# Kernel optimization log

Measured on AMD Instinct MI355X. Metric: run time of the kernel, lower is better.

The kernel has to match this reference:

```python
import jax, jax.numpy as jnp
import numpy as np
import math

CHANNELS, BINS, HEADS, KSIZE = 4, 1024, 8, 3
ROT_DIM = BINS // HEADS // 2  # 64: rotate first half of each 128-dim head


def _rope(t):
    # t: [b, c, heads, w, d]; rotate first ROT_DIM dims, interleaved-pair style
    w = t.shape[-2]
    inv_freq = 1.0 / (10000.0 ** (jnp.arange(0, ROT_DIM, 2, dtype=jnp.float32) / ROT_DIM))
    freqs = jnp.arange(w, dtype=jnp.float32)[:, None] * inv_freq[None, :]   # [w, ROT_DIM//2]
    freqs = jnp.repeat(freqs, 2, axis=-1)                                    # [w, ROT_DIM]
    cos, sin = jnp.cos(freqs), jnp.sin(freqs)
    t_rot, t_pass = t[..., :ROT_DIM], t[..., ROT_DIM:]
    pair = t_rot.reshape(t_rot.shape[:-1] + (ROT_DIM // 2, 2))
    rotated = jnp.stack((-pair[..., 1], pair[..., 0]), axis=-1).reshape(t_rot.shape)
    return jnp.concatenate([t_rot * cos + rotated * sin, t_pass], axis=-1)


def _proj(x, w_lin, w_conv, b_conv):
    # MultichannelLinear: contract last dim with per-channel [out, in] weight
    y = jnp.einsum('bchi,coi->bcho', x, w_lin)
    # depthwise Conv2d, kernel (1, 3), padding (0, 1), groups = channels
    y = jax.lax.conv_general_dilated(
        y, w_conv, window_strides=(1, 1), padding=((0, 0), (1, 1)),
        dimension_numbers=('NCHW', 'OIHW', 'NCHW'), feature_group_count=CHANNELS)
    return y + b_conv[None, :, None, None]


def _split_heads(y):
    b, c, h, w = y.shape
    # transpose(2,3) -> [b,c,w,h]; reshape -> [b,c,w,heads,d]; permute -> [b,c,heads,w,d]
    return y.transpose(0, 1, 3, 2).reshape(b, c, w, HEADS, h // HEADS).transpose(0, 1, 3, 2, 4)


def setup_inputs() -> dict:
    key = jax.random.key(0)
    k1, k2, k3, k4, k5 = jax.random.split(key, 5)
    s_lin = 1.0 / math.sqrt(BINS)
    x = jax.random.normal(k1, (2, CHANNELS, BINS, BINS), dtype=jnp.float32)
    w_q_lin = jax.random.uniform(k2, (CHANNELS, BINS, BINS), jnp.float32, -s_lin, s_lin)
    w_q_conv = jax.random.uniform(k3, (CHANNELS, 1, 1, KSIZE), jnp.float32, -0.5, 0.5)
    b_q_conv = jax.random.uniform(k4, (CHANNELS,), jnp.float32, -0.5, 0.5)
    w_out = jax.random.uniform(k5, (CHANNELS, BINS, BINS), jnp.float32, -s_lin, s_lin)
    return {"x": x, "w_q_lin": w_q_lin, "w_q_conv": w_q_conv, "b_q_conv": b_q_conv, "w_out": w_out}


def reference(x, w_q_lin, w_q_conv, b_q_conv, w_out):
    b, c, h, w = x.shape
    # NOTE: original forward uses self.q_proj for q, k AND v (k_proj/v_proj unused)
    p = _proj(x, w_q_lin, w_q_conv, b_q_conv)          # [b,c,h,w]
    ph = _split_heads(p)                                # [b,c,heads,w,d]
    q = _rope(ph)
    k = _rope(ph)
    v = ph
    qk = jnp.einsum('bcnqd,bcnkd->bcnqk', q, k) / math.sqrt(h)
    a = jnp.einsum('bcnqk,bcnkd->bcnqd', jax.nn.softmax(qk, axis=-1), v)
    # merge heads back: [b,c,heads,w,d] -> [b,c,w,h] -> [b,c,h,w]
    a = a.transpose(0, 1, 3, 2, 4).reshape(b, c, w, h).transpose(0, 1, 3, 2)
    return jnp.einsum('bchi,coi->bcho', a, w_out)
```

## Files before the change

### kernel.cpp

```cpp
#include <hip/hip_runtime.h>
#include <cstdint>
#include <cstddef>

typedef __bf16 bf16;
typedef bf16 bf16x4 __attribute__((ext_vector_type(4)));
typedef bf16 bf16x8 __attribute__((ext_vector_type(8)));
typedef float f32x4 __attribute__((ext_vector_type(4)));

__device__ __forceinline__ void gload_lds16(const bf16* g, bf16* l) {
    __builtin_amdgcn_global_load_lds(
        (__attribute__((address_space(1))) void*)(uintptr_t)(g),
        (__attribute__((address_space(3))) void*)(l),
        16, 0, 0);
}

__global__ __launch_bounds__(256) void cvt_kernel(const float* __restrict__ in,
                                                  bf16* __restrict__ out, int n4) {
    int i = blockIdx.x * 256 + threadIdx.x;
    if (i >= n4) return;
    float4 v = ((const float4*)in)[i];
    bf16x4 o;
    o[0] = (bf16)v.x; o[1] = (bf16)v.y; o[2] = (bf16)v.z; o[3] = (bf16)v.w;
    *(bf16x4*)(out + (size_t)i * 4) = o;
}

__global__ __launch_bounds__(256) void rope_tab_kernel(float2* __restrict__ t) {
    int i = blockIdx.x * 256 + threadIdx.x;
    int w = i >> 5, j = i & 31;
    float inv = exp2f(-(float)j * (13.287712379549449f / 32.0f));
    float a = (float)w * inv;
    t[i] = make_float2(cosf(a), sinf(a));
}

template <bool F32OUT>
__global__ void __launch_bounds__(256) gemm_bt(const bf16* __restrict__ A,
                                               const bf16* __restrict__ B,
                                               void* __restrict__ Cout) {
    __shared__ alignas(16) bf16 As[128 * 64];
    __shared__ alignas(16) bf16 Bs[128 * 64];
    const int tid = threadIdx.x, lane = tid & 63, wave = tid >> 6;
    const int l15 = lane & 15, quad = lane >> 4;
    const int s = blockIdx.z;
    const bf16* Ab = A + ((size_t)s << 20) + (size_t)blockIdx.y * 128 * 1024;
    const bf16* Bb = B + ((size_t)(s & 3) << 20) + (size_t)blockIdx.x * 128 * 1024;
    const int wm = (wave >> 1) * 64, wn = (wave & 1) * 64;

    const f32x4 fzero = {0.f, 0.f, 0.f, 0.f};
    f32x4 acc[4][4];
    for (int i = 0; i < 4; ++i)
        for (int j = 0; j < 4; ++j) acc[i][j] = fzero;

    const int sr = wave * 8 + (lane >> 3);
    const int sc = (lane & 7) * 8;

    for (int kt = 0; kt < 16; ++kt) {
        __syncthreads();
        for (int it = 0; it < 4; ++it) {
            int r = it * 32 + sr;
            gload_lds16(Ab + (size_t)r * 1024 + kt * 64 + sc, As + r * 64 + sc);
            gload_lds16(Bb + (size_t)r * 1024 + kt * 64 + sc, Bs + r * 64 + sc);
        }
        __syncthreads();
        for (int kk = 0; kk < 2; ++kk) {
            bf16x8 af[4], bfr[4];
            for (int i = 0; i < 4; ++i)
                af[i] = *(const bf16x8*)(As + (wm + i * 16 + l15) * 64 + kk * 32 + quad * 8);
            for (int j = 0; j < 4; ++j)
                bfr[j] = *(const bf16x8*)(Bs + (wn + j * 16 + l15) * 64 + kk * 32 + quad * 8);
            for (int i = 0; i < 4; ++i)
                for (int j = 0; j < 4; ++j)
                    acc[i][j] = __builtin_amdgcn_mfma_f32_16x16x32_bf16(af[i], bfr[j],
                                                                        acc[i][j], 0, 0, 0);
        }
    }
    size_t cbase = ((size_t)s << 20) + (size_t)blockIdx.y * 128 * 1024 + blockIdx.x * 128;
    for (int i = 0; i < 4; ++i)
        for (int j = 0; j < 4; ++j) {
            int m = wm + i * 16 + quad * 4;
            int n = wn + j * 16 + l15;
            for (int r = 0; r < 4; ++r) {
                float v = acc[i][j][r];
                if (F32OUT)
                    ((float*)Cout)[cbase + (size_t)(m + r) * 1024 + n] = v;
                else
                    ((bf16*)Cout)[cbase + (size_t)(m + r) * 1024 + n] = (bf16)v;
            }
        }
}

__global__ void __launch_bounds__(256) conv_rope_kernel(
    const bf16* __restrict__ Yb, const float* __restrict__ wconv,
    const float* __restrict__ bconv, bf16* __restrict__ Qhat,
    bf16* __restrict__ Vhat, const float2* __restrict__ rtab) {
    __shared__ float Pt[32][260];
    const int s = blockIdx.z, cch = s & 3;
    const int h0 = blockIdx.y * 32, w0 = blockIdx.x * 256;
    const bf16* Y = Yb + ((size_t)s << 20);
    const float k0 = wconv[cch * 3], k1 = wconv[cch * 3 + 1], k2 = wconv[cch * 3 + 2];
    const float bias = bconv[cch];

    for (int it = 0; it < 4; ++it) {
        const int hh = threadIdx.x >> 3;
        const int wseg = (threadIdx.x & 7) + it * 8;
        const int h = h0 + hh, w = w0 + wseg * 8;
        const bf16* yrow = Y + ((size_t)h << 10);
        bf16x8 yv = *(const bf16x8*)(yrow + w);
        float yc[10];
        yc[0] = (w > 0) ? (float)yrow[w - 1] : 0.f;
        for (int i = 0; i < 8; ++i) yc[i + 1] = (float)yv[i];
        yc[9] = (w + 8 < 1024) ? (float)yrow[w + 8] : 0.f;
        bf16x8 pb;
        for (int i = 0; i < 8; ++i) {
            float p = fmaf(k0, yc[i], fmaf(k1, yc[i + 1], fmaf(k2, yc[i + 2], bias)));
            Pt[hh][wseg * 8 + i] = p;
            pb[i] = (bf16)p;
        }
        const int head = h >> 7, d = h & 127;
        *(bf16x8*)(Vhat + ((((size_t)s * 8 + head) * 128 + (w >> 3)) << 10) + d * 8) = pb;
    }
    __syncthreads();
    {
        const int dcb = threadIdx.x >> 6;
        const int head = h0 >> 7;
        const int d0 = (h0 & 127) + dcb * 8;
        const int hb0 = dcb * 8;
        for (int it = 0; it < 4; ++it) {
            const int wl = (threadIdx.x & 63) + it * 64;
            const int w = w0 + wl;
            float q[8];
            if (d0 < 64) {
                for (int j = 0; j < 8; j += 2) {
                    float2 cs = rtab[(w << 5) + ((d0 + j) >> 1)];
                    float a = Pt[hb0 + j][wl], b = Pt[hb0 + j + 1][wl];
                    q[j]     = fmaf(a, cs.x, -b * cs.y);
                    q[j + 1] = fmaf(b, cs.x,  a * cs.y);
                }
            } else {
                for (int j = 0; j < 8; ++j) q[j] = Pt[hb0 + j][wl];
            }
            bf16x8 qb;
            for (int j = 0; j < 8; ++j) qb[j] = (bf16)q[j];
            *(bf16x8*)(Qhat + ((((size_t)s * 8 + head) * 16 + (d0 >> 3)) << 13) +
                       (size_t)w * 8) = qb;
        }
    }
}

__global__ void __launch_bounds__(256, 2) attn_kernel(const bf16* __restrict__ Qhat,
                                                      const bf16* __restrict__ Vhat,
                                                      bf16* __restrict__ AO) {
    __shared__ alignas(16) char smem[51200];
    bf16* Ks = (bf16*)smem;
    bf16* Vs = (bf16*)(smem + 16384);
    bf16* Ps = (bf16*)(smem + 32768);

    const int tid = threadIdx.x, lane = tid & 63, wave = tid >> 6;
    const int l15 = lane & 15, quad = lane >> 4;
    const int b = blockIdx.x + blockIdx.y * 8 + blockIdx.z * 64;
    const int sh = b & 63, qtile = b >> 6;
    const int s = sh >> 3, head = sh & 7, q0 = qtile * 128;
    const bf16* Qg = Qhat + (size_t)sh * 131072;
    const bf16* Vg = Vhat + (size_t)sh * 131072;

    bf16x8 qf[2][4];
    for (int i = 0; i < 2; ++i)
        for (int kk = 0; kk < 4; ++kk)
            qf[i][kk] = *(const bf16x8*)(Qg + (size_t)(kk * 4 + quad) * 8192 +
                                         (size_t)(q0 + wave * 32 + i * 16 + l15) * 8);

    const f32x4 fzero = {0.f, 0.f, 0.f, 0.f};
    f32x4 Oacc[2][8];
    for (int i = 0; i < 2; ++i)
        for (int j = 0; j < 8; ++j) Oacc[i][j] = fzero;
    float lsum[2][4];
    for (int i = 0; i < 2; ++i)
        for (int r = 0; r < 4; ++r) lsum[i][r] = 0.f;

    const float cexp = 1.4426950408889634f / 32.0f;
    bf16* myP = Ps + wave * (32 * 72);

    for (int kt = 0; kt < 16; ++kt) {
        __syncthreads();
        for (int t = 0; t < 4; ++t) {
            int dc = wave * 4 + t;
            gload_lds16(Qg + (size_t)dc * 8192 + (size_t)(kt * 64 + lane) * 8,
                        Ks + (dc * 64 + lane) * 8);
            int wc = dc >> 1, half = dc & 1;
            gload_lds16(Vg + (size_t)(kt * 8 + wc) * 1024 + (size_t)(half * 64 + lane) * 8,
                        Vs + (wc * 128 + half * 64 + lane) * 8);
        }
        __syncthreads();

        f32x4 sacc[2][4];
        for (int i = 0; i < 2; ++i)
            for (int j = 0; j < 4; ++j) sacc[i][j] = fzero;
        for (int kk = 0; kk < 4; ++kk) {
            bf16x8 kf[4];
            for (int j = 0; j < 4; ++j)
                kf[j] = *(const bf16x8*)(Ks + ((kk * 4 + quad) * 64 + j * 16 + l15) * 8);
            for (int i = 0; i < 2; ++i)
                for (int j = 0; j < 4; ++j)
                    sacc[i][j] = __builtin_amdgcn_mfma_f32_16x16x32_bf16(qf[i][kk], kf[j],
                                                                         sacc[i][j], 0, 0, 0);
        }
        for (int i = 0; i < 2; ++i)
            for (int r = 0; r < 4; ++r) {
                float acc = 0.f;
                for (int j = 0; j < 4; ++j) {
                    float p = exp2f(sacc[i][j][r] * cexp);
                    myP[(i * 16 + quad * 4 + r) * 72 + j * 16 + l15] = (bf16)p;
                    acc += p;
                }
                lsum[i][r] += acc;
            }
        for (int kk2 = 0; kk2 < 2; ++kk2) {
            bf16x8 pf[2];
            for (int i = 0; i < 2; ++i)
                pf[i] = *(const bf16x8*)(myP + (i * 16 + l15) * 72 + kk2 * 32 + quad * 8);
            for (int j = 0; j < 8; ++j) {
                bf16x8 vf = *(const bf16x8*)(Vs + ((kk2 * 4 + quad) * 128 + j * 16 + l15) * 8);
                for (int i = 0; i < 2; ++i)
                    Oacc[i][j] = __builtin_amdgcn_mfma_f32_16x16x32_bf16(pf[i], vf,
                                                                         Oacc[i][j], 0, 0, 0);
            }
        }
    }

    float rinv[2][4];
    for (int i = 0; i < 2; ++i)
        for (int r = 0; r < 4; ++r) {
            float v = lsum[i][r];
            v += __shfl_xor(v, 1);
            v += __shfl_xor(v, 2);
            v += __shfl_xor(v, 4);
            v += __shfl_xor(v, 8);
            rinv[i][r] = 1.0f / v;
        }
    __syncthreads();
    bf16* Ot = (bf16*)smem;
    for (int i = 0; i < 2; ++i)
        for (int j = 0; j < 8; ++j)
            for (int r = 0; r < 4; ++r) {
                int q = wave * 32 + i * 16 + quad * 4 + r;
                int d = j * 16 + l15;
                Ot[d * 136 + q] = (bf16)(Oacc[i][j][r] * rinv[i][r]);
            }
    __syncthreads();
    bf16* AOg = AO + ((size_t)s << 20);
    for (int it = 0; it < 8; ++it) {
        int d = it * 16 + (tid >> 4);
        int qc = (tid & 15) * 8;
        bf16x8 v = *(const bf16x8*)(Ot + d * 136 + qc);
        *(bf16x8*)(AOg + (size_t)(head * 128 + d) * 1024 + q0 + qc) = v;
    }
}

extern "C" void kernel_launch(void* const* d_in, const int* in_sizes, int n_in,
                              void* d_out, int out_size, void* d_ws, size_t ws_size,
                              hipStream_t stream) {
    const float* x  = (const float*)d_in[0];
    const float* wq = (const float*)d_in[1];
    const float* wc = (const float*)d_in[2];
    const float* bc = (const float*)d_in[3];
    const float* wo = (const float*)d_in[4];
    float* out = (float*)d_out;

    char* ws = (char*)d_ws;
    bf16* xb   = (bf16*)ws;
    bf16* wqb  = (bf16*)(ws + (16u << 20));
    bf16* wob  = (bf16*)(ws + (24u << 20));
    bf16* Yb   = (bf16*)(ws + (32u << 20));
    bf16* Qhat = (bf16*)(ws + (48u << 20));
    bf16* Vhat = (bf16*)(ws + (64u << 20));
    float2* rtab = (float2*)(ws + (80u << 20));
    bf16* AO   = xb;

    cvt_kernel<<<8192, 256, 0, stream>>>(x, xb, 2097152);
    cvt_kernel<<<4096, 256, 0, stream>>>(wq, wqb, 1048576);
    cvt_kernel<<<4096, 256, 0, stream>>>(wo, wob, 1048576);
    rope_tab_kernel<<<128, 256, 0, stream>>>(rtab);

    gemm_bt<false><<<dim3(8, 8, 8), 256, 0, stream>>>(xb, wqb, Yb);
    conv_rope_kernel<<<dim3(4, 32, 8), 256, 0, stream>>>(Yb, wc, bc, Qhat, Vhat, rtab);
    attn_kernel<<<dim3(8, 8, 8), 256, 0, stream>>>(Qhat, Vhat, AO);
    gemm_bt<true><<<dim3(8, 8, 8), 256, 0, stream>>>(AO, wob, out);
}
```

Baseline: 233.1 us.

## Double-buffer K/V in attention, widen query tile to 256, transpose QK MFMA

The attention kernel now handles 256 queries per block (64 per wave) instead of 128, which halves how many times K/V tiles are reloaded. K/V staging is double-buffered so the async global-to-LDS load of the next tile overlaps compute on the current one. The QK^T MFMA operands are swapped so P is produced transposed, which allows packed bf16x4 LDS stores and a simpler row-sum reduction. In exchange, the grid drops to 256 blocks at one block per CU, with larger LDS and register use, which lowers occupancy and may leave some CUs idle.

```diff
diff --git a/kernel.cpp b/kernel.cpp
--- a/kernel.cpp
+++ b/kernel.cpp
@@ -146,41 +146,38 @@
     }
 }
 
-__global__ void __launch_bounds__(256, 2) attn_kernel(const bf16* __restrict__ Qhat,
+__global__ void __launch_bounds__(256, 1) attn_kernel(const bf16* __restrict__ Qhat,
                                                       const bf16* __restrict__ Vhat,
                                                       bf16* __restrict__ AO) {
-    __shared__ alignas(16) char smem[51200];
-    bf16* Ks = (bf16*)smem;
-    bf16* Vs = (bf16*)(smem + 16384);
-    bf16* Ps = (bf16*)(smem + 32768);
-
+    __shared__ alignas(16) char smem[102400];
     const int tid = threadIdx.x, lane = tid & 63, wave = tid >> 6;
     const int l15 = lane & 15, quad = lane >> 4;
-    const int b = blockIdx.x + blockIdx.y * 8 + blockIdx.z * 64;
+    const int b = blockIdx.x;
     const int sh = b & 63, qtile = b >> 6;
-    const int s = sh >> 3, head = sh & 7, q0 = qtile * 128;
+    const int s = sh >> 3, head = sh & 7;
+    const int q0 = qtile * 256;
     const bf16* Qg = Qhat + (size_t)sh * 131072;
     const bf16* Vg = Vhat + (size_t)sh * 131072;
-
-    bf16x8 qf[2][4];
-    for (int i = 0; i < 2; ++i)
+    bf16* myP = (bf16*)(smem + 65536) + wave * (64 * 72);
+
+    bf16x8 qf[4][4];
+    for (int i = 0; i < 4; ++i)
         for (int kk = 0; kk < 4; ++kk)
             qf[i][kk] = *(const bf16x8*)(Qg + (size_t)(kk * 4 + quad) * 8192 +
-                                         (size_t)(q0 + wave * 32 + i * 16 + l15) * 8);
+                                         (size_t)(q0 + wave * 64 + i * 16 + l15) * 8);
 
     const f32x4 fzero = {0.f, 0.f, 0.f, 0.f};
-    f32x4 Oacc[2][8];
-    for (int i = 0; i < 2; ++i)
+    f32x4 Oacc[4][8];
+    for (int i = 0; i < 4; ++i)
         for (int j = 0; j < 8; ++j) Oacc[i][j] = fzero;
-    float lsum[2][4];
-    for (int i = 0; i < 2; ++i)
-        for (int r = 0; r < 4; ++r) lsum[i][r] = 0.f;
+    float lsum[4];
+    for (int i = 0; i < 4; ++i) lsum[i] = 0.f;
 
     const float cexp = 1.4426950408889634f / 32.0f;
-    bf16* myP = Ps + wave * (32 * 72);
-
-    for (int kt = 0; kt < 16; ++kt) {
-        __syncthreads();
+
+    auto stage = [&](int kt, int buf) {
+        bf16* Ks = (bf16*)(smem + buf * 32768);
+        bf16* Vs = Ks + 8192;
         for (int t = 0; t < 4; ++t) {
             int dc = wave * 4 + t;
             gload_lds16(Qg + (size_t)dc * 8192 + (size_t)(kt * 64 + lane) * 8,
@@ -189,68 +186,79 @@
             gload_lds16(Vg + (size_t)(kt * 8 + wc) * 1024 + (size_t)(half * 64 + lane) * 8,
                         Vs + (wc * 128 + half * 64 + lane) * 8);
         }
+    };
+
+    stage(0, 0);
+    for (int kt = 0; kt < 16; ++kt) {
         __syncthreads();
-
-        f32x4 sacc[2][4];
-        for (int i = 0; i < 2; ++i)
-            for (int j = 0; j < 4; ++j) sacc[i][j] = fzero;
+        if (kt < 15) stage(kt + 1, (kt + 1) & 1);
+        bf16* Ks = (bf16*)(smem + (kt & 1) * 32768);
+        bf16* Vs = Ks + 8192;
+
+        f32x4 st[4][4];
+        for (int jt = 0; jt < 4; ++jt)
+            for (int i = 0; i < 4; ++i) st[jt][i] = fzero;
         for (int kk = 0; kk < 4; ++kk) {
             bf16x8 kf[4];
-            for (int j = 0; j < 4; ++j)
-                kf[j] = *(const bf16x8*)(Ks + ((kk * 4 + quad) * 64 + j * 16 + l15) * 8);
-            for (int i = 0; i < 2; ++i)
-                for (int j = 0; j < 4; ++j)
-                    sacc[i][j] = __builtin_amdgcn_mfma_f32_16x16x32_bf16(qf[i][kk], kf[j],
-                                                                         sacc[i][j], 0, 0, 0);
-        }
-        for (int i = 0; i < 2; ++i)
-            for (int r = 0; r < 4; ++r) {
-                float acc = 0.f;
-                for (int j = 0; j < 4; ++j) {
-                    float p = exp2f(sacc[i][j][r] * cexp);
-                    myP[(i * 16 + quad * 4 + r) * 72 + j * 16 + l15] = (bf16)p;
+            for (int jt = 0; jt < 4; ++jt)
+                kf[jt] = *(const bf16x8*)(Ks + ((kk * 4 + quad) * 64 + jt * 16 + l15) * 8);
+            for (int jt = 0; jt < 4; ++jt)
+                for (int i = 0; i < 4; ++i)
+                    st[jt][i] = __builtin_amdgcn_mfma_f32_16x16x32_bf16(kf[jt], qf[i][kk],
+                                                                       st[jt][i], 0, 0, 0);
+        }
+        for (int i = 0; i < 4; ++i) {
+            float acc = 0.f;
+            for (int jt = 0; jt < 4; ++jt) {
+                bf16x4 pk;
+                for (int r = 0; r < 4; ++r) {
+                    float p = exp2f(st[jt][i][r] * cexp);
+                    pk[r] = (bf16)p;
                     acc += p;
                 }
-                lsum[i][r] += acc;
-            }
+                *(bf16x4*)(myP + (i * 16 + l15) * 72 + jt * 16 + quad * 4) = pk;
+            }
+            lsum[i] += acc;
+        }
         for (int kk2 = 0; kk2 < 2; ++kk2) {
-            bf16x8 pf[2];
-            for (int i = 0; i < 2; ++i)
+            bf16x8 pf[4];
+            for (int i = 0; i < 4; ++i)
                 pf[i] = *(const bf16x8*)(myP + (i * 16 + l15) * 72 + kk2 * 32 + quad * 8);
             for (int j = 0; j < 8; ++j) {
                 bf16x8 vf = *(const bf16x8*)(Vs + ((kk2 * 4 + quad) * 128 + j * 16 + l15) * 8);
-                for (int i = 0; i < 2; ++i)
+                for (int i = 0; i < 4; ++i)
                     Oacc[i][j] = __builtin_amdgcn_mfma_f32_16x16x32_bf16(pf[i], vf,
                                                                          Oacc[i][j], 0, 0, 0);
             }
         }
     }
 
-    float rinv[2][4];
-    for (int i = 0; i < 2; ++i)
-        for (int r = 0; r < 4; ++r) {
-            float v = lsum[i][r];
-            v += __shfl_xor(v, 1);
-            v += __shfl_xor(v, 2);
-            v += __shfl_xor(v, 4);
-            v += __shfl_xor(v, 8);
-            rinv[i][r] = 1.0f / v;
-        }
+    float* lsf = (float*)myP;
+    for (int i = 0; i < 4; ++i) {
+        float v = lsum[i];
+        v += __shfl_xor(v, 16);
+        v += __shfl_xor(v, 32);
+        lsf[i * 16 + l15] = v;
+    }
+    float rinv[4][4];
+    for (int i = 0; i < 4; ++i)
+        for (int r = 0; r < 4; ++r) rinv[i][r] = 1.0f / lsf[i * 16 + quad * 4 + r];
+
     __syncthreads();
     bf16* Ot = (bf16*)smem;
-    for (int i = 0; i < 2; ++i)
+    for (int i = 0; i < 4; ++i)
         for (int j = 0; j < 8; ++j)
             for (int r = 0; r < 4; ++r) {
-                int q = wave * 32 + i * 16 + quad * 4 + r;
+                int q = wave * 64 + i * 16 + quad * 4 + r;
                 int d = j * 16 + l15;
-                Ot[d * 136 + q] = (bf16)(Oacc[i][j][r] * rinv[i][r]);
+                Ot[d * 264 + q] = (bf16)(Oacc[i][j][r] * rinv[i][r]);
             }
     __syncthreads();
     bf16* AOg = AO + ((size_t)s << 20);
-    for (int it = 0; it < 8; ++it) {
-        int d = it * 16 + (tid >> 4);
-        int qc = (tid & 15) * 8;
-        bf16x8 v = *(const bf16x8*)(Ot + d * 136 + qc);
+    for (int it = 0; it < 16; ++it) {
+        int d = it * 8 + (tid >> 5);
+        int qc = (tid & 31) * 8;
+        bf16x8 v = *(const bf16x8*)(Ot + d * 264 + qc);
         *(bf16x8*)(AOg + (size_t)(head * 128 + d) * 1024 + q0 + qc) = v;
     }
 }
@@ -282,6 +290,6 @@
 
     gemm_bt<false><<<dim3(8, 8, 8), 256, 0, stream>>>(xb, wqb, Yb);
     conv_rope_kernel<<<dim3(4, 32, 8), 256, 0, stream>>>(Yb, wc, bc, Qhat, Vhat, rtab);
-    attn_kernel<<<dim3(8, 8, 8), 256, 0, stream>>>(Qhat, Vhat, AO);
+    attn_kernel<<<256, 256, 0, stream>>>(Qhat, Vhat, AO);
     gemm_bt<true><<<dim3(8, 8, 8), 256, 0, stream>>>(AO, wob, out);
 }
```

Result: slower. 242.5 us (+4.0%).

## Rewrite attention with 32x32 MFMA, register-resident P and double-buffered K/V

Applied to the files above, without the earlier changes.

The attention kernel moves from 16x16x32 to 32x32x16 bf16 MFMA and computes S transposed, so the exponentiated probabilities stay in registers. They are packed to bf16 pairs and exchanged across half-waves with shuffles instead of being written to and read back from LDS. K/V tiles are now double-buffered in LDS, so the next tile's global-to-LDS load overlaps the current compute and one barrier per iteration is removed. LDS use grows to about 66KB per block, which may limit occupancy at two blocks per CU, and the shuffle-based P layout adds register pressure.

```diff
diff --git a/kernel.cpp b/kernel.cpp
--- a/kernel.cpp
+++ b/kernel.cpp
@@ -3,9 +3,13 @@
 #include <cstddef>
 
 typedef __bf16 bf16;
+typedef bf16 bf16x2 __attribute__((ext_vector_type(2)));
 typedef bf16 bf16x4 __attribute__((ext_vector_type(4)));
 typedef bf16 bf16x8 __attribute__((ext_vector_type(8)));
 typedef float f32x4 __attribute__((ext_vector_type(4)));
+typedef float f32x16 __attribute__((ext_vector_type(16)));
+
+union B2F { float f; bf16x2 h; };
 
 __device__ __forceinline__ void gload_lds16(const bf16* g, bf16* l) {
     __builtin_amdgcn_global_load_lds(
@@ -149,38 +153,30 @@
 __global__ void __launch_bounds__(256, 2) attn_kernel(const bf16* __restrict__ Qhat,
                                                       const bf16* __restrict__ Vhat,
                                                       bf16* __restrict__ AO) {
-    __shared__ alignas(16) char smem[51200];
-    bf16* Ks = (bf16*)smem;
-    bf16* Vs = (bf16*)(smem + 16384);
-    bf16* Ps = (bf16*)(smem + 32768);
-
+    __shared__ alignas(16) char smem[66048];
     const int tid = threadIdx.x, lane = tid & 63, wave = tid >> 6;
-    const int l15 = lane & 15, quad = lane >> 4;
-    const int b = blockIdx.x + blockIdx.y * 8 + blockIdx.z * 64;
+    const int l31 = lane & 31, h = lane >> 5;
+    const int b = blockIdx.x;
     const int sh = b & 63, qtile = b >> 6;
     const int s = sh >> 3, head = sh & 7, q0 = qtile * 128;
     const bf16* Qg = Qhat + (size_t)sh * 131072;
     const bf16* Vg = Vhat + (size_t)sh * 131072;
 
-    bf16x8 qf[2][4];
-    for (int i = 0; i < 2; ++i)
-        for (int kk = 0; kk < 4; ++kk)
-            qf[i][kk] = *(const bf16x8*)(Qg + (size_t)(kk * 4 + quad) * 8192 +
-                                         (size_t)(q0 + wave * 32 + i * 16 + l15) * 8);
-
-    const f32x4 fzero = {0.f, 0.f, 0.f, 0.f};
-    f32x4 Oacc[2][8];
-    for (int i = 0; i < 2; ++i)
-        for (int j = 0; j < 8; ++j) Oacc[i][j] = fzero;
-    float lsum[2][4];
-    for (int i = 0; i < 2; ++i)
-        for (int r = 0; r < 4; ++r) lsum[i][r] = 0.f;
+    const int myq = q0 + wave * 32 + l31;
+    bf16x8 qf[8];
+    for (int ks8 = 0; ks8 < 8; ++ks8)
+        qf[ks8] = *(const bf16x8*)(Qg + (size_t)(ks8 * 2 + h) * 8192 + (size_t)myq * 8);
+
+    f32x16 Oacc[4];
+    for (int nt = 0; nt < 4; ++nt)
+        for (int e = 0; e < 16; ++e) Oacc[nt][e] = 0.f;
+    float lsum = 0.f;
 
     const float cexp = 1.4426950408889634f / 32.0f;
-    bf16* myP = Ps + wave * (32 * 72);
-
-    for (int kt = 0; kt < 16; ++kt) {
-        __syncthreads();
+
+    auto stage = [&](int kt, int buf) {
+        bf16* Ks = (bf16*)(smem + buf * 32768);
+        bf16* Vs = Ks + 8192;
         for (int t = 0; t < 4; ++t) {
             int dc = wave * 4 + t;
             gload_lds16(Qg + (size_t)dc * 8192 + (size_t)(kt * 64 + lane) * 8,
@@ -189,62 +185,73 @@
             gload_lds16(Vg + (size_t)(kt * 8 + wc) * 1024 + (size_t)(half * 64 + lane) * 8,
                         Vs + (wc * 128 + half * 64 + lane) * 8);
         }
+    };
+
+    stage(0, 0);
+    for (int kt = 0; kt < 16; ++kt) {
         __syncthreads();
-
-        f32x4 sacc[2][4];
-        for (int i = 0; i < 2; ++i)
-            for (int j = 0; j < 4; ++j) sacc[i][j] = fzero;
-        for (int kk = 0; kk < 4; ++kk) {
-            bf16x8 kf[4];
-            for (int j = 0; j < 4; ++j)
-                kf[j] = *(const bf16x8*)(Ks + ((kk * 4 + quad) * 64 + j * 16 + l15) * 8);
-            for (int i = 0; i < 2; ++i)
-                for (int j = 0; j < 4; ++j)
-                    sacc[i][j] = __builtin_amdgcn_mfma_f32_16x16x32_bf16(qf[i][kk], kf[j],
-                                                                         sacc[i][j], 0, 0, 0);
-        }
-        for (int i = 0; i < 2; ++i)
-            for (int r = 0; r < 4; ++r) {
-                float acc = 0.f;
-                for (int j = 0; j < 4; ++j) {
-                    float p = exp2f(sacc[i][j][r] * cexp);
-                    myP[(i * 16 + quad * 4 + r) * 72 + j * 16 + l15] = (bf16)p;
-                    acc += p;
-                }
-                lsum[i][r] += acc;
-            }
-        for (int kk2 = 0; kk2 < 2; ++kk2) {
-            bf16x8 pf[2];
-            for (int i = 0; i < 2; ++i)
-                pf[i] = *(const bf16x8*)(myP + (i * 16 + l15) * 72 + kk2 * 32 + quad * 8);
-            for (int j = 0; j < 8; ++j) {
-                bf16x8 vf = *(const bf16x8*)(Vs + ((kk2 * 4 + quad) * 128 + j * 16 + l15) * 8);
-                for (int i = 0; i < 2; ++i)
-                    Oacc[i][j] = __builtin_amdgcn_mfma_f32_16x16x32_bf16(pf[i], vf,
-                                                                         Oacc[i][j], 0, 0, 0);
-            }
-        }
-    }
-
-    float rinv[2][4];
-    for (int i = 0; i < 2; ++i)
-        for (int r = 0; r < 4; ++r) {
-            float v = lsum[i][r];
-            v += __shfl_xor(v, 1);
-            v += __shfl_xor(v, 2);
-            v += __shfl_xor(v, 4);
-            v += __shfl_xor(v, 8);
-            rinv[i][r] = 1.0f / v;
-        }
+        if (kt < 15) stage(kt + 1, (kt + 1) & 1);
+        bf16* Ks = (bf16*)(smem + (kt & 1) * 32768);
+        bf16* Vs = Ks + 8192;
+
+        f32x16 st[2];
+        for (int e = 0; e < 16; ++e) { st[0][e] = 0.f; st[1][e] = 0.f; }
+        for (int ks8 = 0; ks8 < 8; ++ks8) {
+            bf16x8 kf0 = *(const bf16x8*)(Ks + ((ks8 * 2 + h) * 64 + l31) * 8);
+            bf16x8 kf1 = *(const bf16x8*)(Ks + ((ks8 * 2 + h) * 64 + 32 + l31) * 8);
+            st[0] = __builtin_amdgcn_mfma_f32_32x32x16_bf16(kf0, qf[ks8], st[0], 0, 0, 0);
+            st[1] = __builtin_amdgcn_mfma_f32_32x32x16_bf16(kf1, qf[ks8], st[1], 0, 0, 0);
+        }
+
+        float pk[2][8], pkx[2][8];
+        float lacc = 0.f;
+        for (int mt = 0; mt < 2; ++mt)
+            for (int k = 0; k < 8; ++k) {
+                float a = exp2f(st[mt][2 * k] * cexp);
+                float c = exp2f(st[mt][2 * k + 1] * cexp);
+                lacc += a + c;
+                B2F u; u.h = bf16x2{(bf16)a, (bf16)c};
+                pk[mt][k] = u.f;
+            }
+        lsum += lacc;
+        for (int mt = 0; mt < 2; ++mt)
+            for (int k = 0; k < 8; ++k) pkx[mt][k] = __shfl_xor(pk[mt][k], 32);
+
+        for (int ks = 0; ks < 4; ++ks) {
+            const int bb = ks & 1, mt = ks >> 1;
+            bf16x8 pf;
+            float* pfF = (float*)&pf;
+            pfF[0] = h ? pkx[mt][4 * bb + 2] : pk[mt][4 * bb + 0];
+            pfF[1] = h ? pkx[mt][4 * bb + 3] : pk[mt][4 * bb + 1];
+            pfF[2] = h ? pk[mt][4 * bb + 2] : pkx[mt][4 * bb + 0];
+            pfF[3] = h ? pk[mt][4 * bb + 3] : pkx[mt][4 * bb + 1];
+            for (int nt = 0; nt < 4; ++nt) {
+                bf16x8 vf = *(const bf16x8*)(Vs + ((ks * 2 + h) * 128 + nt * 32 + l31) * 8);
+                Oacc[nt] = __builtin_amdgcn_mfma_f32_32x32x16_bf16(pf, vf, Oacc[nt], 0, 0, 0);
+            }
+        }
+    }
+
+    lsum += __shfl_xor(lsum, 32);
+    float* lsf = (float*)(smem + 65536) + wave * 32;
+    if (lane < 32) lsf[lane] = 1.0f / lsum;
+    f32x4 rv[4];
+    __builtin_amdgcn_s_waitcnt(0);
+    for (int rg = 0; rg < 4; ++rg)
+        rv[rg] = *(const f32x4*)(lsf + 8 * rg + 4 * h);
+
     __syncthreads();
     bf16* Ot = (bf16*)smem;
-    for (int i = 0; i < 2; ++i)
-        for (int j = 0; j < 8; ++j)
-            for (int r = 0; r < 4; ++r) {
-                int q = wave * 32 + i * 16 + quad * 4 + r;
-                int d = j * 16 + l15;
-                Ot[d * 136 + q] = (bf16)(Oacc[i][j][r] * rinv[i][r]);
-            }
+    for (int nt = 0; nt < 4; ++nt) {
+        int d = nt * 32 + l31;
+        for (int rg = 0; rg < 4; ++rg) {
+            int q = wave * 32 + 8 * rg + 4 * h;
+            bf16x4 o4;
+            for (int e = 0; e < 4; ++e)
+                o4[e] = (bf16)(Oacc[nt][rg * 4 + e] * rv[rg][e]);
+            *(bf16x4*)(Ot + d * 136 + q) = o4;
+        }
+    }
     __syncthreads();
     bf16* AOg = AO + ((size_t)s << 20);
     for (int it = 0; it < 8; ++it) {
@@ -282,6 +289,6 @@
 
     gemm_bt<false><<<dim3(8, 8, 8), 256, 0, stream>>>(xb, wqb, Yb);
     conv_rope_kernel<<<dim3(4, 32, 8), 256, 0, stream>>>(Yb, wc, bc, Qhat, Vhat, rtab);
-    attn_kernel<<<dim3(8, 8, 8), 256, 0, stream>>>(Qhat, Vhat, AO);
+    attn_kernel<<<512, 256, 0, stream>>>(Qhat, Vhat, AO);
     gemm_bt<true><<<dim3(8, 8, 8), 256, 0, stream>>>(AO, wob, out);
 }
```

Result: faster. 227.5 us (-2.4%).
